# Kernel tuning notes

Measured on AMD Instinct MI355X. Metric: run time of the kernel, lower is better.

The kernel has to match this reference:

```python
import jax, jax.numpy as jnp
import numpy as np

N_NODES = 50000
N_EDGES = 1600000
NODE_F = 92
EDGE_F = 41
HID = 128
N_CONV = 3
N_GRAPHS = 256
OUT_DIM = 1


def setup_inputs() -> dict:
    key = jax.random.key(0)
    ks = jax.random.split(key, 16)
    s = 0.05
    x = jax.random.normal(ks[0], (N_NODES, NODE_F), dtype=jnp.float32)
    edge_index = jax.random.randint(ks[1], (2, N_EDGES), 0, N_NODES, dtype=jnp.int64)
    edge_attr = jax.random.normal(ks[2], (N_EDGES, EDGE_F), dtype=jnp.float32)
    batch = jnp.sort(jax.random.randint(ks[3], (N_NODES,), 0, N_GRAPHS, dtype=jnp.int64))
    zdim = 2 * HID + EDGE_F
    return {
        "x": x,
        "edge_index": edge_index,
        "edge_attr": edge_attr,
        "batch": batch,
        "emb_w": jax.random.normal(ks[4], (NODE_F, HID), dtype=jnp.float32) * s,
        "emb_b": jnp.zeros((HID,), dtype=jnp.float32),
        "msg_w": jax.random.normal(ks[5], (N_CONV, zdim, HID), dtype=jnp.float32) * s,
        "msg_b": jnp.zeros((N_CONV, HID), dtype=jnp.float32),
        "gate_w": jax.random.normal(ks[6], (N_CONV, zdim, HID), dtype=jnp.float32) * s,
        "gate_b": jnp.zeros((N_CONV, HID), dtype=jnp.float32),
        "ro1_w": jax.random.normal(ks[7], (HID, HID), dtype=jnp.float32) * s,
        "ro1_b": jnp.zeros((HID,), dtype=jnp.float32),
        "ro2_w": jax.random.normal(ks[8], (HID, OUT_DIM), dtype=jnp.float32) * s,
        "ro2_b": jnp.zeros((OUT_DIM,), dtype=jnp.float32),
    }


def _conv(x, edge_index, edge_attr, wm, bm, wg, bg):
    # edge_index[0] = target (i), edge_index[1] = source (j) per PyG convention
    dst, src = edge_index[0], edge_index[1]
    x_i = x[dst]                              # [E, H]
    x_j = x[src]                              # [E, H]
    z = jnp.concatenate([x_i, x_j, edge_attr], axis=1)  # [E, 2H+Fe]
    gate = jax.nn.sigmoid(z @ wm + bm)        # message_mlp (Sigmoid)
    msg = jax.nn.softplus(z @ wg + bg)        # gate_mlp (Softplus)
    contrib = gate * msg                      # [E, H]
    aggr = jax.ops.segment_sum(contrib, dst, num_segments=x.shape[0])
    return jax.nn.softplus(x + aggr)


def reference(x, edge_index, edge_attr, batch, emb_w, emb_b,
              msg_w, msg_b, gate_w, gate_b, ro1_w, ro1_b, ro2_w, ro2_b):
    h = x @ emb_w + emb_b
    for l in range(N_CONV):
        h = _conv(h, edge_index, edge_attr, msg_w[l], msg_b[l], gate_w[l], gate_b[l])
    # scatter mean over graphs
    sums = jax.ops.segment_sum(h, batch, num_segments=N_GRAPHS)
    cnt = jax.ops.segment_sum(jnp.ones((h.shape[0], 1), h.dtype), batch, num_segments=N_GRAPHS)
    pooled = sums / jnp.maximum(cnt, 1.0)
    out = jax.nn.softplus(pooled @ ro1_w + ro1_b) @ ro2_w + ro2_b
    return out
```

## Files before the change

### kernel.cpp

```cpp
#include <hip/hip_runtime.h>
#include <hip/hip_bf16.h>
#include <math.h>

#define NNODES 50000
#define NEDGES 1600000
#define NODEF 92
#define EDGEF 41
#define HID 128
#define NCONV 3
#define NGRAPHS 256
#define ZDIM 297
#define KPAD 320
#define KSTEPS 10
#define ZLD 328
#define ME 32

typedef _Float16 half8 __attribute__((ext_vector_type(8)));
typedef _Float16 half4 __attribute__((ext_vector_type(4)));
typedef float f32x4 __attribute__((ext_vector_type(4)));

__device__ __forceinline__ float softplus_f(float x) {
    return fmaxf(x, 0.f) + __logf(1.f + __expf(-fabsf(x)));
}
__device__ __forceinline__ float sigmoid_f(float x) {
    return __builtin_amdgcn_rcpf(1.f + __expf(-x));
}

__global__ void prep_wfrag(const float* __restrict__ msg_w, const float* __restrict__ gate_w,
                           half8* __restrict__ wf) {
    const int idx = blockIdx.x * blockDim.x + threadIdx.x;
    const int total = NCONV * 16 * KSTEPS * 64;
    if (idx >= total) return;
    const int lane = idx & 63;
    const int rest = idx >> 6;
    const int ks = rest % KSTEPS;
    const int gl = rest / KSTEPS;
    const int g = gl & 15;
    const int l = gl >> 4;
    const int branch = g & 1;
    const int j = (g >> 2) * 32 + ((g >> 1) & 1) * 16 + (lane & 15);
    const int k0 = ks * 32 + (lane >> 4) * 8;
    const float* W = branch ? gate_w : msg_w;
    half8 v;
    #pragma unroll
    for (int jj = 0; jj < 8; ++jj) {
        const int k = k0 + jj;
        const float f = (k < ZDIM) ? W[((size_t)l * ZDIM + k) * HID + j] : 0.f;
        v[jj] = (_Float16)f;
    }
    wf[idx] = v;
}

__global__ void embed_kernel(const float* __restrict__ x, const float* __restrict__ w,
                             const float* __restrict__ b, float* __restrict__ h) {
    __shared__ float xs[NODEF];
    const int n = blockIdx.x;
    const int j = threadIdx.x;
    if (j < NODEF) xs[j] = x[(size_t)n * NODEF + j];
    __syncthreads();
    float acc = b[j];
    #pragma unroll 4
    for (int k = 0; k < NODEF; ++k) acc = fmaf(xs[k], w[k * HID + j], acc);
    h[(size_t)n * HID + j] = acc;
}

__global__ __launch_bounds__(256) void edge_mfma_kernel(
    const float* __restrict__ h, const int* __restrict__ ei,
    const float* __restrict__ ea, const half8* __restrict__ wf,
    const float* __restrict__ bm, const float* __restrict__ bg,
    float* __restrict__ aggr) {
    __shared__ __align__(16) _Float16 zs[ME][ZLD];
    __shared__ const float4* shp[2 * ME];
    __shared__ float* sbase[ME];

    const int t = threadIdx.x;
    const int eb = blockIdx.x * ME;
    if (t < ME) {
        const int d = ei[eb + t];
        shp[t] = (const float4*)(h + (size_t)d * HID);
        sbase[t] = aggr + (size_t)d * HID;
    } else if (t < 2 * ME) {
        shp[t] = (const float4*)(h + (size_t)ei[NEDGES + eb + (t - ME)] * HID);
    }
    __syncthreads();

    #pragma unroll
    for (int i = 0; i < 8; ++i) {
        const int idx = t + 256 * i;
        const int r = idx >> 6;
        const int c4 = idx & 63;
        const float4 v = (c4 < 32) ? shp[r][c4] : shp[ME + r][c4 - 32];
        *(half4*)&zs[r][c4 * 4] = (half4){(_Float16)v.x, (_Float16)v.y,
                                          (_Float16)v.z, (_Float16)v.w};
    }
    #pragma unroll
    for (int i = 0; i < 8; ++i) {
        const int idx = t + 256 * i;
        const int r = idx >> 6;
        const int k = 256 + (idx & 63);
        float f = 0.f;
        if (k < ZDIM) f = ea[(size_t)(eb + r) * EDGEF + (k - 256)];
        zs[r][k] = (_Float16)f;
    }
    __syncthreads();

    const int wave = t >> 6;
    const int lane = t & 63;
    const int arow = lane & 15;
    const int koff = (lane >> 4) * 8;

    f32x4 acc[2][4];
    #pragma unroll
    for (int m = 0; m < 2; ++m)
        #pragma unroll
        for (int n = 0; n < 4; ++n) acc[m][n] = (f32x4){0.f, 0.f, 0.f, 0.f};

    const half8* wfw = wf + (size_t)(wave * 4) * KSTEPS * 64 + lane;
    #pragma unroll 2
    for (int ks = 0; ks < KSTEPS; ++ks) {
        const int kb = ks * 32 + koff;
        const half8 a0 = *(const half8*)&zs[arow][kb];
        const half8 a1 = *(const half8*)&zs[16 + arow][kb];
        #pragma unroll
        for (int nt = 0; nt < 4; ++nt) {
            const half8 b = wfw[(size_t)(nt * KSTEPS + ks) * 64];
            acc[0][nt] = __builtin_amdgcn_mfma_f32_16x16x32_f16(a0, b, acc[0][nt], 0, 0, 0);
            acc[1][nt] = __builtin_amdgcn_mfma_f32_16x16x32_f16(a1, b, acc[1][nt], 0, 0, 0);
        }
    }

    const int j0 = wave * 32 + (lane & 15);
    const float bm0 = bm[j0], bm1 = bm[j0 + 16];
    const float bg0 = bg[j0], bg1 = bg[j0 + 16];
    #pragma unroll
    for (int m = 0; m < 2; ++m) {
        #pragma unroll
        for (int r = 0; r < 4; ++r) {
            const int row = m * 16 + (lane >> 4) * 4 + r;
            float* base = sbase[row];
            {
                const float gate = sigmoid_f(acc[m][0][r] + bm0);
                const float msg = softplus_f(acc[m][1][r] + bg0);
                atomicAdd(base + j0, gate * msg);
            }
            {
                const float gate = sigmoid_f(acc[m][2][r] + bm1);
                const float msg = softplus_f(acc[m][3][r] + bg1);
                atomicAdd(base + j0 + 16, gate * msg);
            }
        }
    }
}

__global__ void update_kernel(float* __restrict__ h, const float* __restrict__ aggr) {
    const size_t idx = (size_t)blockIdx.x * blockDim.x + threadIdx.x;
    float4 hv = ((const float4*)h)[idx];
    const float4 av = ((const float4*)aggr)[idx];
    hv.x = softplus_f(hv.x + av.x);
    hv.y = softplus_f(hv.y + av.y);
    hv.z = softplus_f(hv.z + av.z);
    hv.w = softplus_f(hv.w + av.w);
    ((float4*)h)[idx] = hv;
}

__global__ void readout_kernel(const float* __restrict__ h, const int* __restrict__ batch,
                               const float* __restrict__ ro1w, const float* __restrict__ ro1b,
                               const float* __restrict__ ro2w, const float* __restrict__ ro2b,
                               float* __restrict__ out) {
    __shared__ float pooled[HID];
    __shared__ float red[HID];
    __shared__ int range[2];
    const int g = blockIdx.x, j = threadIdx.x;
    if (j == 0) {
        int lo = 0, hi = NNODES;
        while (lo < hi) { int mid = (lo + hi) >> 1; if (batch[mid] < g) lo = mid + 1; else hi = mid; }
        range[0] = lo;
        hi = NNODES;
        while (lo < hi) { int mid = (lo + hi) >> 1; if (batch[mid] < g + 1) lo = mid + 1; else hi = mid; }
        range[1] = lo;
    }
    __syncthreads();
    const int start = range[0], end = range[1];
    float s = 0.f;
    for (int n = start; n < end; ++n) s += h[(size_t)n * HID + j];
    const float cnt = (float)(end - start);
    pooled[j] = s / fmaxf(cnt, 1.f);
    __syncthreads();
    float acc = ro1b[j];
    #pragma unroll 4
    for (int k = 0; k < HID; ++k) acc = fmaf(pooled[k], ro1w[k * HID + j], acc);
    red[j] = softplus_f(acc) * ro2w[j];
    __syncthreads();
    for (int sdt = 64; sdt > 0; sdt >>= 1) {
        if (j < sdt) red[j] += red[j + sdt];
        __syncthreads();
    }
    if (j == 0) out[g] = red[0] + ro2b[0];
}

extern "C" void kernel_launch(void* const* d_in, const int* in_sizes, int n_in,
                              void* d_out, int out_size, void* d_ws, size_t ws_size,
                              hipStream_t stream) {
    (void)in_sizes; (void)n_in; (void)out_size; (void)ws_size;
    const float* x      = (const float*)d_in[0];
    const int*   ei     = (const int*)d_in[1];
    const float* ea     = (const float*)d_in[2];
    const int*   batch  = (const int*)d_in[3];
    const float* emb_w  = (const float*)d_in[4];
    const float* emb_b  = (const float*)d_in[5];
    const float* msg_w  = (const float*)d_in[6];
    const float* msg_b  = (const float*)d_in[7];
    const float* gate_w = (const float*)d_in[8];
    const float* gate_b = (const float*)d_in[9];
    const float* ro1w   = (const float*)d_in[10];
    const float* ro1b   = (const float*)d_in[11];
    const float* ro2w   = (const float*)d_in[12];
    const float* ro2b   = (const float*)d_in[13];
    float* out = (float*)d_out;

    float* ws   = (float*)d_ws;
    float* h    = ws;
    float* aggr = h + (size_t)NNODES * HID;
    half8* wfrag = (half8*)(aggr + (size_t)NNODES * HID);

    const int wtotal = NCONV * 16 * KSTEPS * 64;
    prep_wfrag<<<(wtotal + 255) / 256, 256, 0, stream>>>(msg_w, gate_w, wfrag);
    embed_kernel<<<NNODES, HID, 0, stream>>>(x, emb_w, emb_b, h);

    for (int l = 0; l < NCONV; ++l) {
        hipMemsetAsync(aggr, 0, (size_t)NNODES * HID * sizeof(float), stream);
        edge_mfma_kernel<<<NEDGES / ME, 256, 0, stream>>>(
            h, ei, ea, wfrag + (size_t)l * 16 * KSTEPS * 64,
            msg_b + l * HID, gate_b + l * HID, aggr);
        update_kernel<<<(NNODES * HID / 4) / 256, 256, 0, stream>>>(h, aggr);
    }

    readout_kernel<<<NGRAPHS, HID, 0, stream>>>(h, batch, ro1w, ro1b, ro2w, ro2b, out);
}
```

Measured before the change: 3.030 ms.

## Precompute per-node dst projection and sort edges by destination for segmented reduction

```diff
diff --git a/kernel.cpp b/kernel.cpp
--- a/kernel.cpp
+++ b/kernel.cpp
@@ -10,10 +10,13 @@
 #define NCONV 3
 #define NGRAPHS 256
 #define ZDIM 297
-#define KPAD 320
 #define KSTEPS 10
-#define ZLD 328
+#define KS0 4
+#define NKS 6
 #define ME 32
+#define ZLD2 200
+#define NLD 136
+#define CLD 132
 
 typedef _Float16 half8 __attribute__((ext_vector_type(8)));
 typedef _Float16 half4 __attribute__((ext_vector_type(4)));
@@ -24,6 +27,52 @@
 }
 __device__ __forceinline__ float sigmoid_f(float x) {
     return __builtin_amdgcn_rcpf(1.f + __expf(-x));
+}
+
+__global__ void hist_kernel(const int* __restrict__ ei, int* __restrict__ cnt) {
+    const int e = blockIdx.x * blockDim.x + threadIdx.x;
+    if (e < NEDGES) atomicAdd(&cnt[ei[e]], 1);
+}
+
+#define SCAN_T 1024
+__global__ __launch_bounds__(1024) void scan_kernel(const int* __restrict__ cnt,
+                                                    int* __restrict__ cursor) {
+    __shared__ int part[SCAN_T];
+    const int tid = threadIdx.x;
+    const int chunk = (NNODES + SCAN_T - 1) / SCAN_T;
+    const int base = tid * chunk;
+    int s = 0;
+    for (int i = 0; i < chunk; ++i) {
+        const int idx = base + i;
+        if (idx < NNODES) s += cnt[idx];
+    }
+    part[tid] = s;
+    __syncthreads();
+    for (int off = 1; off < SCAN_T; off <<= 1) {
+        int v = 0;
+        if (tid >= off) v = part[tid - off];
+        __syncthreads();
+        part[tid] += v;
+        __syncthreads();
+    }
+    int run = part[tid] - s;
+    for (int i = 0; i < chunk; ++i) {
+        const int idx = base + i;
+        if (idx < NNODES) { cursor[idx] = run; run += cnt[idx]; }
+    }
+}
+
+__global__ void scatter_kernel(const int* __restrict__ ei, int* __restrict__ cursor,
+                               int* __restrict__ perm, int* __restrict__ dstS,
+                               int* __restrict__ srcS) {
+    const int e = blockIdx.x * blockDim.x + threadIdx.x;
+    if (e < NEDGES) {
+        const int d = ei[e];
+        const int p = atomicAdd(&cursor[d], 1);
+        perm[p] = e;
+        dstS[p] = d;
+        srcS[p] = ei[NEDGES + e];
+    }
 }
 
 __global__ void prep_wfrag(const float* __restrict__ msg_w, const float* __restrict__ gate_w,
@@ -64,63 +113,37 @@
     h[(size_t)n * HID + j] = acc;
 }
 
-__global__ __launch_bounds__(256) void edge_mfma_kernel(
-    const float* __restrict__ h, const int* __restrict__ ei,
-    const float* __restrict__ ea, const half8* __restrict__ wf,
+__global__ __launch_bounds__(256) void node_pre_kernel(
+    const float* __restrict__ h, const half8* __restrict__ wf,
     const float* __restrict__ bm, const float* __restrict__ bg,
-    float* __restrict__ aggr) {
-    __shared__ __align__(16) _Float16 zs[ME][ZLD];
-    __shared__ const float4* shp[2 * ME];
-    __shared__ float* sbase[ME];
-
+    float* __restrict__ nprec) {
+    __shared__ __align__(16) _Float16 zn[32][NLD];
     const int t = threadIdx.x;
-    const int eb = blockIdx.x * ME;
-    if (t < ME) {
-        const int d = ei[eb + t];
-        shp[t] = (const float4*)(h + (size_t)d * HID);
-        sbase[t] = aggr + (size_t)d * HID;
-    } else if (t < 2 * ME) {
-        shp[t] = (const float4*)(h + (size_t)ei[NEDGES + eb + (t - ME)] * HID);
-    }
-    __syncthreads();
-
-    #pragma unroll
-    for (int i = 0; i < 8; ++i) {
+    const int nb = blockIdx.x * 32;
+    #pragma unroll
+    for (int i = 0; i < 4; ++i) {
         const int idx = t + 256 * i;
-        const int r = idx >> 6;
-        const int c4 = idx & 63;
-        const float4 v = (c4 < 32) ? shp[r][c4] : shp[ME + r][c4 - 32];
-        *(half4*)&zs[r][c4 * 4] = (half4){(_Float16)v.x, (_Float16)v.y,
+        const int r = idx >> 5;
+        const int c4 = idx & 31;
+        const int n = (nb + r < NNODES) ? nb + r : NNODES - 1;
+        const float4 v = ((const float4*)(h + (size_t)n * HID))[c4];
+        *(half4*)&zn[r][c4 * 4] = (half4){(_Float16)v.x, (_Float16)v.y,
                                           (_Float16)v.z, (_Float16)v.w};
     }
-    #pragma unroll
-    for (int i = 0; i < 8; ++i) {
-        const int idx = t + 256 * i;
-        const int r = idx >> 6;
-        const int k = 256 + (idx & 63);
-        float f = 0.f;
-        if (k < ZDIM) f = ea[(size_t)(eb + r) * EDGEF + (k - 256)];
-        zs[r][k] = (_Float16)f;
-    }
-    __syncthreads();
-
-    const int wave = t >> 6;
-    const int lane = t & 63;
-    const int arow = lane & 15;
-    const int koff = (lane >> 4) * 8;
-
+    __syncthreads();
+    const int wave = t >> 6, lane = t & 63;
+    const int arow = lane & 15, koff = (lane >> 4) * 8;
     f32x4 acc[2][4];
     #pragma unroll
     for (int m = 0; m < 2; ++m)
         #pragma unroll
         for (int n = 0; n < 4; ++n) acc[m][n] = (f32x4){0.f, 0.f, 0.f, 0.f};
-
     const half8* wfw = wf + (size_t)(wave * 4) * KSTEPS * 64 + lane;
-    #pragma unroll 2
-    for (int ks = 0; ks < KSTEPS; ++ks) {
+    #pragma unroll
+    for (int ks = 0; ks < 4; ++ks) {
         const int kb = ks * 32 + koff;
-        const half8 a0 = *(const half8*)&zs[arow][kb];
-        const half8 a1 = *(const half8*)&zs[16 + arow][kb];
+        const half8 a0 = *(const half8*)&zn[arow][kb];
+        const half8 a1 = *(const half8*)&zn[16 + arow][kb];
         #pragma unroll
         for (int nt = 0; nt < 4; ++nt) {
             const half8 b = wfw[(size_t)(nt * KSTEPS + ks) * 64];
@@ -128,28 +151,123 @@
             acc[1][nt] = __builtin_amdgcn_mfma_f32_16x16x32_f16(a1, b, acc[1][nt], 0, 0, 0);
         }
     }
+    const int l15 = lane & 15;
+    #pragma unroll
+    for (int nt = 0; nt < 4; ++nt) {
+        const int branch = nt & 1;
+        const int j = wave * 32 + ((nt >> 1) & 1) * 16 + l15;
+        const float bias = branch ? bg[j] : bm[j];
+        const int col = branch * 128 + j;
+        #pragma unroll
+        for (int m = 0; m < 2; ++m)
+            #pragma unroll
+            for (int r = 0; r < 4; ++r) {
+                const int n = nb + m * 16 + ((lane >> 4) & 3) * 4 + r;
+                if (n < NNODES) nprec[(size_t)n * 256 + col] = acc[m][nt][r] + bias;
+            }
+    }
+}
+
+__global__ __launch_bounds__(256) void edge_mfma_kernel(
+    const float* __restrict__ h, const int* __restrict__ dstS, const int* __restrict__ srcS,
+    const int* __restrict__ perm, const float* __restrict__ ea, const half8* __restrict__ wf,
+    const float* __restrict__ nprec, float* __restrict__ aggr) {
+    __shared__ __align__(16) unsigned char smem_u[32 * CLD * 4];
+    __shared__ const float4* ssrcp[ME];
+    __shared__ const float* seap[ME];
+    __shared__ const float* snp[ME];
+    __shared__ int sdstv[ME];
+
+    _Float16 (*zs)[ZLD2] = (_Float16(*)[ZLD2])smem_u;
+    float* cont = (float*)smem_u;
+
+    const int t = threadIdx.x;
+    const int eb = blockIdx.x * ME;
+    if (t < ME) {
+        const int d = dstS[eb + t];
+        sdstv[t] = d;
+        snp[t] = nprec + (size_t)d * 256;
+    } else if (t < 2 * ME) {
+        ssrcp[t - ME] = (const float4*)(h + (size_t)srcS[eb + t - ME] * HID);
+    } else if (t < 3 * ME) {
+        seap[t - 2 * ME] = ea + (size_t)perm[eb + t - 2 * ME] * EDGEF;
+    }
+    __syncthreads();
+
+    #pragma unroll
+    for (int i = 0; i < 4; ++i) {
+        const int idx = t + 256 * i;
+        const int r = idx >> 5;
+        const int c4 = idx & 31;
+        const float4 v = ssrcp[r][c4];
+        *(half4*)&zs[r][c4 * 4] = (half4){(_Float16)v.x, (_Float16)v.y,
+                                          (_Float16)v.z, (_Float16)v.w};
+    }
+    #pragma unroll
+    for (int i = 0; i < 8; ++i) {
+        const int idx = t + 256 * i;
+        const int r = idx >> 6;
+        const int kk = idx & 63;
+        const float f = (kk < EDGEF) ? seap[r][kk] : 0.f;
+        zs[r][128 + kk] = (_Float16)f;
+    }
+    __syncthreads();
+
+    const int wave = t >> 6, lane = t & 63;
+    const int arow = lane & 15, koff = (lane >> 4) * 8;
+    f32x4 acc[2][4];
+    #pragma unroll
+    for (int m = 0; m < 2; ++m)
+        #pragma unroll
+        for (int n = 0; n < 4; ++n) acc[m][n] = (f32x4){0.f, 0.f, 0.f, 0.f};
+
+    const half8* wfw = wf + (size_t)(wave * 4) * KSTEPS * 64 + lane;
+    #pragma unroll
+    for (int ks = 0; ks < NKS; ++ks) {
+        const int kb = ks * 32 + koff;
+        const half8 a0 = *(const half8*)&zs[arow][kb];
+        const half8 a1 = *(const half8*)&zs[16 + arow][kb];
+        #pragma unroll
+        for (int nt = 0; nt < 4; ++nt) {
+            const half8 b = wfw[(size_t)(nt * KSTEPS + KS0 + ks) * 64];
+            acc[0][nt] = __builtin_amdgcn_mfma_f32_16x16x32_f16(a0, b, acc[0][nt], 0, 0, 0);
+            acc[1][nt] = __builtin_amdgcn_mfma_f32_16x16x32_f16(a1, b, acc[1][nt], 0, 0, 0);
+        }
+    }
+    __syncthreads();
 
     const int j0 = wave * 32 + (lane & 15);
-    const float bm0 = bm[j0], bm1 = bm[j0 + 16];
-    const float bg0 = bg[j0], bg1 = bg[j0 + 16];
     #pragma unroll
     for (int m = 0; m < 2; ++m) {
         #pragma unroll
         for (int r = 0; r < 4; ++r) {
             const int row = m * 16 + (lane >> 4) * 4 + r;
-            float* base = sbase[row];
-            {
-                const float gate = sigmoid_f(acc[m][0][r] + bm0);
-                const float msg = softplus_f(acc[m][1][r] + bg0);
-                atomicAdd(base + j0, gate * msg);
-            }
-            {
-                const float gate = sigmoid_f(acc[m][2][r] + bm1);
-                const float msg = softplus_f(acc[m][3][r] + bg1);
-                atomicAdd(base + j0 + 16, gate * msg);
-            }
+            const float* np = snp[row];
+            const float g0 = sigmoid_f(acc[m][0][r] + np[j0]);
+            const float s0 = softplus_f(acc[m][1][r] + np[128 + j0]);
+            cont[row * CLD + j0] = g0 * s0;
+            const float g1 = sigmoid_f(acc[m][2][r] + np[j0 + 16]);
+            const float s1 = softplus_f(acc[m][3][r] + np[128 + j0 + 16]);
+            cont[row * CLD + j0 + 16] = g1 * s1;
         }
     }
+    __syncthreads();
+
+    const int c = t & 127;
+    const int r0 = (t >> 7) * 16;
+    float s = cont[r0 * CLD + c];
+    int prev = sdstv[r0];
+    #pragma unroll
+    for (int r = r0 + 1; r < r0 + 16; ++r) {
+        const int d = sdstv[r];
+        if (d != prev) {
+            atomicAdd(&aggr[(size_t)prev * HID + c], s);
+            s = 0.f;
+            prev = d;
+        }
+        s += cont[r * CLD + c];
+    }
+    atomicAdd(&aggr[(size_t)prev * HID + c], s);
 }
 
 __global__ void update_kernel(float* __restrict__ h, const float* __restrict__ aggr) {
@@ -218,20 +336,34 @@
     const float* ro2b   = (const float*)d_in[13];
     float* out = (float*)d_out;
 
-    float* ws   = (float*)d_ws;
-    float* h    = ws;
-    float* aggr = h + (size_t)NNODES * HID;
-    half8* wfrag = (half8*)(aggr + (size_t)NNODES * HID);
+    char* wsb = (char*)d_ws;
+    float* h     = (float*)wsb;                 wsb += (size_t)NNODES * HID * 4;
+    float* aggr  = (float*)wsb;                 wsb += (size_t)NNODES * HID * 4;
+    float* nprec = (float*)wsb;                 wsb += (size_t)NNODES * 256 * 4;
+    half8* wfrag = (half8*)wsb;                 wsb += (size_t)NCONV * 16 * KSTEPS * 64 * 16;
+    int* cnt     = (int*)wsb;                   wsb += (size_t)NNODES * 4;
+    int* cursor  = (int*)wsb;                   wsb += (size_t)NNODES * 4;
+    int* perm    = (int*)wsb;                   wsb += (size_t)NEDGES * 4;
+    int* dstS    = (int*)wsb;                   wsb += (size_t)NEDGES * 4;
+    int* srcS    = (int*)wsb;                   wsb += (size_t)NEDGES * 4;
+
+    hipMemsetAsync(cnt, 0, (size_t)NNODES * 4, stream);
+    hist_kernel<<<NEDGES / 256, 256, 0, stream>>>(ei, cnt);
+    scan_kernel<<<1, SCAN_T, 0, stream>>>(cnt, cursor);
+    scatter_kernel<<<NEDGES / 256, 256, 0, stream>>>(ei, cursor, perm, dstS, srcS);
 
     const int wtotal = NCONV * 16 * KSTEPS * 64;
     prep_wfrag<<<(wtotal + 255) / 256, 256, 0, stream>>>(msg_w, gate_w, wfrag);
     embed_kernel<<<NNODES, HID, 0, stream>>>(x, emb_w, emb_b, h);
 
     for (int l = 0; l < NCONV; ++l) {
-        hipMemsetAsync(aggr, 0, (size_t)NNODES * HID * sizeof(float), stream);
+        hipMemsetAsync(aggr, 0, (size_t)NNODES * HID * 4, stream);
+        node_pre_kernel<<<(NNODES + 31) / 32, 256, 0, stream>>>(
+            h, wfrag + (size_t)l * 16 * KSTEPS * 64,
+            msg_b + l * HID, gate_b + l * HID, nprec);
         edge_mfma_kernel<<<NEDGES / ME, 256, 0, stream>>>(
-            h, ei, ea, wfrag + (size_t)l * 16 * KSTEPS * 64,
-            msg_b + l * HID, gate_b + l * HID, aggr);
+            h, dstS, srcS, perm, ea, wfrag + (size_t)l * 16 * KSTEPS * 64,
+            nprec, aggr);
         update_kernel<<<(NNODES * HID / 4) / 256, 256, 0, stream>>>(h, aggr);
     }
 
```

Result: slower. 3.273 ms (+8.0%).
